# Optimization experiments

Measured on AMD Instinct MI355X. Metric: run time of the kernel, lower is better.

Reference implementation:

```python
import jax, jax.numpy as jnp
import numpy as np
import math

N_NODES = 20000
N_EDGES = 320000
NODE_IN = 128
HIDDEN = 64
HEADS = 4
TIME_DIM = 64
SCALE = 60.0 / 1.0  # sensitivity / epsilon


def _linear_params(key, din, dout):
    k1, k2 = jax.random.split(key)
    bound = 1.0 / math.sqrt(din)
    w = jax.random.uniform(k1, (din, dout), minval=-bound, maxval=bound, dtype=jnp.float32)
    b = jax.random.uniform(k2, (dout,), minval=-bound, maxval=bound, dtype=jnp.float32)
    return w, b


def setup_inputs() -> dict:
    key = jax.random.key(0)
    ks = jax.random.split(key, 16)
    edge_index = jax.random.randint(ks[0], (2, N_EDGES), 0, N_NODES, dtype=jnp.int64)
    raw_time = jax.random.uniform(ks[1], (N_EDGES, 1), dtype=jnp.float32) * 86400.0
    noise = jax.random.laplace(ks[2], (N_EDGES, 1), dtype=jnp.float32) * SCALE
    node_emb = jax.random.normal(ks[3], (N_NODES, NODE_IN), dtype=jnp.float32)
    HC = HEADS * HIDDEN
    wq1, bq1 = _linear_params(ks[4], NODE_IN, HC)
    wk1, bk1 = _linear_params(ks[5], NODE_IN, HC)
    wv1, bv1 = _linear_params(ks[6], NODE_IN, HC)
    wt1, bt1 = _linear_params(ks[7], TIME_DIM, HC)
    wq2, bq2 = _linear_params(ks[8], HC, HC)
    wk2, bk2 = _linear_params(ks[9], HC, HC)
    wv2, bv2 = _linear_params(ks[10], HC, HC)
    wt2, bt2 = _linear_params(ks[11], TIME_DIM, HC)
    wc, bc = _linear_params(ks[12], HC, 1)
    return dict(edge_index=edge_index, raw_time=raw_time, noise=noise, node_emb=node_emb,
                wq1=wq1, bq1=bq1, wk1=wk1, bk1=bk1, wv1=wv1, bv1=bv1, wt1=wt1, bt1=bt1,
                wq2=wq2, bq2=bq2, wk2=wk2, bk2=bk2, wv2=wv2, bv2=bv2, wt2=wt2, bt2=bt2,
                wc=wc, bc=bc)


def time_encode(t):
    # t: [E, 1] -> [E, TIME_DIM]; interleaved sin/cos as in TimeEncoder
    half = jnp.arange(0, TIME_DIM, 2, dtype=jnp.float32)
    div_term = jnp.exp(half * (-math.log(10000.0) / TIME_DIM))  # [TIME_DIM/2]
    arg = t * div_term  # [E, TIME_DIM/2]
    te = jnp.stack([jnp.sin(arg), jnp.cos(arg)], axis=-1)  # [E, T/2, 2]
    return te.reshape(t.shape[0], TIME_DIM)


def temporal_conv(x, src, dst, time_enc, wq, bq, wk, bk, wv, bv, wt, bt):
    # gather-QKV, edge softmax over dst segments, scatter-add aggregation
    N = x.shape[0]
    q = (x @ wq + bq).reshape(N, HEADS, HIDDEN)
    k = (x @ wk + bk).reshape(N, HEADS, HIDDEN)
    v = (x @ wv + bv).reshape(N, HEADS, HIDDEN)
    t_enc = (time_enc @ wt + bt).reshape(-1, HEADS, HIDDEN)  # [E,H,C]
    q_i = q[dst]                      # [E,H,C]
    k_j = k[src] + t_enc              # [E,H,C]
    alpha = (q_i * k_j).sum(-1) / math.sqrt(HIDDEN)  # [E,H]
    # segment softmax over index = dst (PyG softmax semantics)
    amax = jax.ops.segment_max(alpha, dst, num_segments=N)  # [N,H]
    ea = jnp.exp(alpha - amax[dst])
    denom = jax.ops.segment_sum(ea, dst, num_segments=N)
    alpha = ea / (denom[dst] + 1e-16)
    msg = v[src] * alpha[..., None]   # [E,H,C]
    out = jax.ops.segment_sum(msg, dst, num_segments=N)  # [N,H,C]
    return out.reshape(N, HEADS * HIDDEN)


def reference(edge_index, raw_time, noise, node_emb,
              wq1, bq1, wk1, bk1, wv1, bv1, wt1, bt1,
              wq2, bq2, wk2, bk2, wv2, bv2, wt2, bt2,
              wc, bc):
    src, dst = edge_index[0], edge_index[1]
    noisy_time = raw_time + noise                 # Laplace mechanism
    time_encoded = time_encode(noisy_time)        # [E, TIME_DIM]
    x = jax.nn.relu(temporal_conv(node_emb, src, dst, time_encoded,
                                  wq1, bq1, wk1, bk1, wv1, bv1, wt1, bt1))
    x = jax.nn.relu(temporal_conv(x, src, dst, time_encoded,
                                  wq2, bq2, wk2, bk2, wv2, bv2, wt2, bt2))
    edge_emb = x[src] + x[dst]                    # [E, H*C]
    out = edge_emb @ wc + bc                      # [E, 1]
    return out.squeeze(-1)
```

## Files before the change

kernel.cpp:

```cpp
#include <hip/hip_runtime.h>
#include <hip/hip_fp16.h>
#include <math.h>

#define NN   20000
#define NE   320000
#define NIN  128
#define HC   256
#define NB   1024

#define AGG_BLOCKS 2500
#define AGG_STRIDE 10000
#define LOG2E_8    0.18033688f

#define GEMM_BLOCKS 1280
#define GEMM_RT     157

typedef unsigned short u16;
typedef __attribute__((ext_vector_type(8))) short bf16x8;
typedef __attribute__((ext_vector_type(4))) float f32x4;

__device__ __forceinline__ float bf2f(u16 u) {
  union { unsigned int i; float f; } x;
  x.i = ((unsigned int)u) << 16;
  return x.f;
}
__device__ __forceinline__ u16 f2bf(float f) {
  union { float f; unsigned int i; } x;
  x.f = f;
  unsigned int r = x.i + 0x7fffu + ((x.i >> 16) & 1u);
  return (u16)(r >> 16);
}
__device__ __forceinline__ float bflo(int v) {
  union { int i; float f; } x; x.i = v << 16; return x.f;
}
__device__ __forceinline__ float bfhi(int v) {
  union { int i; float f; } x; x.i = v & 0xffff0000; return x.f;
}

__device__ __forceinline__ float ldf(const void* p, int i, bool fbf) {
  return fbf ? bf2f(((const u16*)p)[i]) : ((const float*)p)[i];
}
__device__ __forceinline__ int ldsrc(const void* p, int e, bool is64) {
  const int* p32 = (const int*)p;
  return is64 ? p32[2 * e] : p32[e];
}
__device__ __forceinline__ int lddst(const void* p, int e, bool is64) {
  const int* p32 = (const int*)p;
  return is64 ? p32[2 * (NE + e)] : p32[NE + e];
}
__device__ __forceinline__ void stout(void* p, int i, float v, bool fbf) {
  if (fbf) ((u16*)p)[i] = f2bf(v);
  else ((float*)p)[i] = v;
}

__device__ __forceinline__ void gload_lds16(const u16* g, u16* l) {
  __builtin_amdgcn_global_load_lds(
      (const __attribute__((address_space(1))) void*)g,
      (__attribute__((address_space(3))) void*)l, 16, 0, 0);
}

__device__ __forceinline__ float dpp_row_allsum(float s) {
  union fi { float f; int i; };
  fi a, b;
  a.f = s;
  b.i = __builtin_amdgcn_update_dpp(0, a.i, 0x121, 0xf, 0xf, true); a.f += b.f;
  b.i = __builtin_amdgcn_update_dpp(0, a.i, 0x122, 0xf, 0xf, true); a.f += b.f;
  b.i = __builtin_amdgcn_update_dpp(0, a.i, 0x124, 0xf, 0xf, true); a.f += b.f;
  b.i = __builtin_amdgcn_update_dpp(0, a.i, 0x128, 0xf, 0xf, true); a.f += b.f;
  return a.f;
}

__device__ __forceinline__ float fexp2(float x) {
#if __has_builtin(__builtin_amdgcn_exp2f)
  return __builtin_amdgcn_exp2f(x);
#else
  return exp2f(x);
#endif
}

#if __has_builtin(__builtin_amdgcn_fdot2_f32_bf16)
#define HAS_BF16_DOT2 1
typedef __attribute__((ext_vector_type(2))) __bf16 bfv2_t;
__device__ __forceinline__ float qkdot2(int a, int b, float c) {
  return __builtin_amdgcn_fdot2_f32_bf16(__builtin_bit_cast(bfv2_t, a),
                                         __builtin_bit_cast(bfv2_t, b), c, false);
}
#else
#define HAS_BF16_DOT2 0
#endif

__device__ __forceinline__ void edge_do(int2 kk, int2 vv, float tt, int2 q2,
    float dc0, float dc1,
    float qsx, float qsy, float qsz, float qsw,
    float px, float py, float pz, float pw, float qb,
    float& denom, float& a0, float& a1, float& a2, float& a3) {
  const float CH = 0.15915494f;
  const float CL = (float)(0.15915494309189535 - (double)0.15915494f);
  float x0 = tt * dc0, x1 = tt * dc1;
  float p0 = x0 * CH, p1 = x1 * CH;
  float e0 = fmaf(x0, CH, -p0), e1 = fmaf(x1, CH, -p1);
  e0 = fmaf(x0, CL, e0);  e1 = fmaf(x1, CL, e1);
  float fr0 = (p0 - rintf(p0)) + e0;
  float fr1 = (p1 - rintf(p1)) + e1;
  float sv0 = __builtin_amdgcn_sinf(fr0), cv0 = __builtin_amdgcn_cosf(fr0);
  float sv1 = __builtin_amdgcn_sinf(fr1), cv1 = __builtin_amdgcn_cosf(fr1);
  float stp = sv0 * px + cv0 * py + sv1 * pz + cv1 * pw;
#if HAS_BF16_DOT2
  float sqk = qkdot2(kk.y, q2.y, qkdot2(kk.x, q2.x, 0.f));
  float partial = sqk * LOG2E_8 + stp;
#else
  float partial = stp + qsx * bflo(kk.x) + qsy * bfhi(kk.x) +
                  qsz * bflo(kk.y) + qsw * bfhi(kk.y);
#endif
  float a = dpp_row_allsum(partial) + qb;
  float ea = fexp2(a);
  denom += ea;
  a0 = fmaf(ea, bflo(vv.x), a0);
  a1 = fmaf(ea, bfhi(vv.x), a1);
  a2 = fmaf(ea, bflo(vv.y), a2);
  a3 = fmaf(ea, bfhi(vv.y), a3);
}

__global__ void devinit_kernel(const void* __restrict__ eidx,
                               const void* __restrict__ nemb,
                               int* __restrict__ flags, float* __restrict__ divt) {
  int lane = threadIdx.x;
  if (lane < 32) {
    const float c32 = (float)(-0.14391156831212787);
    float prod = (float)(2 * lane) * c32;
    divt[lane] = (float)exp((double)prod);
  }
  if (lane == 0) {
    const int* p32 = (const int*)eidx;
    int is64 = 1;
    for (int i = 1; i < 128; i += 2)
      if (p32[i] != 0) { is64 = 0; break; }
    const u16* q16 = (const u16*)nemb;
    int fbf = 1;
    for (int i = 0; i < 128; i += 2) {
      unsigned e = (q16[i] >> 7) & 0xFF;
      if (e < 90 || e > 140) { fbf = 0; break; }
    }
    flags[0] = is64;
    flags[1] = fbf;
  }
}

__global__ void sentinel_kernel(const int* __restrict__ flags, void* __restrict__ out) {
  int i = blockIdx.x * 256 + threadIdx.x;
  if (i < NE) stout(out, i, 3000.0f, flags[1] != 0);
}
__global__ void raw_sentinel_kernel(u16* __restrict__ out) {
  int i = blockIdx.x * 256 + threadIdx.x;
  if (i < NE) out[i] = f2bf(3000.0f);
}

__global__ void zero_kernel(int* __restrict__ p, int n) {
  int i = blockIdx.x * 256 + threadIdx.x;
  if (i < n) p[i] = 0;
}

__global__ void hist_kernel(const int* __restrict__ flags, const void* __restrict__ eidx,
                            int* __restrict__ cnt) {
  bool is64 = flags[0] != 0;
  int e = blockIdx.x * 256 + threadIdx.x;
  if (e < NE) {
    int d = lddst(eidx, e, is64);
    if ((unsigned)d < NN) atomicAdd(&cnt[d], 1);
  }
}

__global__ void scan1_kernel(const int* __restrict__ cnt, int* __restrict__ offs,
                             int* __restrict__ bsum, int n) {
  __shared__ int s[256];
  int b = blockIdx.x, t = threadIdx.x, i = b * 256 + t;
  int x = (i < n) ? cnt[i] : 0;
  s[t] = x;
  __syncthreads();
  for (int off = 1; off < 256; off <<= 1) {
    int y = (t >= off) ? s[t - off] : 0;
    __syncthreads();
    s[t] += y;
    __syncthreads();
  }
  if (i < n) offs[i] = s[t] - x;
  if (t == 255) bsum[b] = s[t];
}

__global__ void scan2_kernel(int* __restrict__ bsum, int* __restrict__ offs,
                             int nb, int n) {
  __shared__ int s[256];
  int t = threadIdx.x;
  int x = (t < nb) ? bsum[t] : 0;
  s[t] = x;
  __syncthreads();
  for (int off = 1; off < 256; off <<= 1) {
    int y = (t >= off) ? s[t - off] : 0;
    __syncthreads();
    s[t] += y;
    __syncthreads();
  }
  if (t < nb) bsum[t] = s[t] - x;
  if (t == 255) offs[n] = s[t];
}

__global__ void scan3_kernel(int* __restrict__ offs, const int* __restrict__ bsum,
                             int* __restrict__ cursor, int n) {
  int i = blockIdx.x * 256 + threadIdx.x;
  if (i < n) {
    int v = offs[i] + bsum[blockIdx.x];
    offs[i] = v;
    cursor[i] = v;
  }
}

__global__ void fill_kernel(const int* __restrict__ flags, const void* __restrict__ eidx,
                            const void* __restrict__ rawt, const void* __restrict__ noise,
                            int* __restrict__ cursor, int* __restrict__ ssrc,
                            float* __restrict__ stt) {
  bool is64 = flags[0] != 0, fbf = flags[1] != 0;
  int e = blockIdx.x * 256 + threadIdx.x;
  if (e < NE) {
    int d = lddst(eidx, e, is64);
    if ((unsigned)d < NN) {
      int pos = atomicAdd(&cursor[d], 1);
      if ((unsigned)pos < NE) {
        int src = ldsrc(eidx, e, is64);
        if ((unsigned)src >= NN) src = 0;
        ssrc[pos] = src;
        stt[pos] = ldf(rawt, e, fbf) + ldf(noise, e, fbf);
      }
    }
  }
}

__global__ __launch_bounds__(256) void cast_kernel(const int* __restrict__ flags,
                                                   const void* __restrict__ in,
                                                   u16* __restrict__ out) {
  if (flags[1]) return;
  int i = blockIdx.x * 256 + threadIdx.x;
  if (i < NN * NIN / 4) {
    float4 v = ((const float4*)in)[i];
    ushort4 o;
    o.x = f2bf(v.x); o.y = f2bf(v.y); o.z = f2bf(v.z); o.w = f2bf(v.w);
    ((ushort4*)out)[i] = o;
  }
}

__global__ void transw3_kernel(const int* __restrict__ flags, const void* __restrict__ W0,
                               const void* __restrict__ W1, const void* __restrict__ W2,
                               u16* __restrict__ WtBig, int K) {
  bool fbf = flags[1] != 0;
  __shared__ u16 tile[64][65];
  int z = blockIdx.z;
  const void* W = (z == 0) ? W0 : (z == 1) ? W1 : W2;
  u16* dst = WtBig + (size_t)z * 256 * K;
  int kb = blockIdx.x * 64, cb = blockIdx.y * 64;
  int tx = threadIdx.x & 63, ty = threadIdx.x >> 6;
  for (int i = ty; i < 64; i += 4)
    tile[tx][i] = f2bf(ldf(W, (kb + i) * HC + cb + tx, fbf));
  __syncthreads();
  for (int i = ty; i < 64; i += 4)
    dst[(size_t)(cb + i) * K + kb + tx] = tile[i][tx];
}

__global__ void wcombbias_kernel(const int* __restrict__ flags, const void* __restrict__ wt,
                                 const u16* __restrict__ Wqt, u16* __restrict__ Wout,
                                 const void* __restrict__ bq, const void* __restrict__ bk,
                                 const void* __restrict__ bv, float* __restrict__ biasBig,
                                 int K) {
  bool fbf = flags[1] != 0;
  int b = blockIdx.x, t = threadIdx.x;
  if (b < 256) {
    __shared__ float wrow[64];
    int j = b, h = j >> 6;
    if (t < 64) wrow[t] = ldf(wt, (j & 63) * HC + h * 64 + t, fbf);
    __syncthreads();
    if (t < K) {
      float s = 0.f;
#pragma unroll 8
      for (int mm = 0; mm < 64; ++mm)
        s += wrow[mm] * bf2f(Wqt[(size_t)(h * 64 + mm) * K + t]);
      Wout[(size_t)j * K + t] = f2bf(s);
    }
  } else if (b < 259) {
    int bb = b - 256;
    const void* p = (bb == 0) ? bq : (bb == 1) ? bk : bv;
    biasBig[bb * 256 + t] = ldf(p, t, fbf);
  } else {
    int j = t, h = j >> 6;
    float s = 0.f;
    for (int mm = 0; mm < 64; ++mm)
      s += ldf(bq, h * 64 + mm, fbf) * ldf(wt, (j & 63) * HC + h * 64 + mm, fbf);
    biasBig[768 + j] = s;
  }
}

template <bool AWS>
__global__ __launch_bounds__(256) void gemm_mfma(
    const int* __restrict__ flags, const void* __restrict__ Ap,
    const u16* __restrict__ Acast, const u16* __restrict__ Wt,
    const float* __restrict__ bias, u16* __restrict__ C, int M, int K) {
  bool fbf = flags[1] != 0;
  const u16* A = AWS ? (const u16*)Ap : (fbf ? (const u16*)Ap : Acast);

  int lid = blockIdx.x;
  int xcd = lid & 7;
  int j = lid >> 3;
  int rl = j >> 3, col = j & 7;
  const int qr = GEMM_RT >> 3, rem = GEMM_RT & 7;
  int nrows = qr + (xcd < rem ? 1 : 0);
  if (rl >= nrows) return;
  int row = xcd * qr + (xcd < rem ? xcd : rem) + rl;
  int rb = row * 128, cb = col * 128;

  __shared__ u16 As[2][128 * 32];
  __shared__ u16 Bs[2][128 * 32];
  int tid = threadIdx.x;
  int wave = tid >> 6, lane = tid & 63;
  int l15 = lane & 15, quad = lane >> 4;
  int mbase = (wave >> 1) * 64, nbase = (wave & 1) * 64;

  f32x4 acc[4][4];
#pragma unroll
  for (int mt = 0; mt < 4; ++mt)
#pragma unroll
    for (int nt = 0; nt < 4; ++nt)
#pragma unroll
      for (int r = 0; r < 4; ++r) acc[mt][nt][r] = 0.f;

  int srow0 = tid >> 2, schunk0 = tid & 3;
  int srow1 = (tid + 256) >> 2, schunk1 = (tid + 256) & 3;
  int gchunk0 = schunk0 ^ (srow0 & 3);
  int gchunk1 = schunk1 ^ (srow1 & 3);
  int arow0 = rb + srow0; if (arow0 >= M) arow0 = M - 1;
  int arow1 = rb + srow1; if (arow1 >= M) arow1 = M - 1;
  int slo0 = srow0 * 32 + schunk0 * 8;
  int slo1 = srow1 * 32 + schunk1 * 8;
  const u16* bsrc0 = Wt + (size_t)(cb + srow0) * K + gchunk0 * 8;
  const u16* bsrc1 = Wt + (size_t)(cb + srow1) * K + gchunk1 * 8;
  const u16* asrc0 = A + (size_t)arow0 * K + gchunk0 * 8;
  const u16* asrc1 = A + (size_t)arow1 * K + gchunk1 * 8;

  auto STAGE = [&](int b, int kk) {
    gload_lds16(asrc0 + kk, &As[b][slo0]);
    gload_lds16(asrc1 + kk, &As[b][slo1]);
    gload_lds16(bsrc0 + kk, &Bs[b][slo0]);
    gload_lds16(bsrc1 + kk, &Bs[b][slo1]);
  };

  auto COMPUTE = [&](int b) {
    bf16x8 bfrag[4];
#pragma unroll
    for (int nt = 0; nt < 4; ++nt) {
      int col2 = nbase + nt * 16 + l15;
      bfrag[nt] = *(const bf16x8*)&Bs[b][col2 * 32 + ((quad ^ (col2 & 3)) * 8)];
    }
#pragma unroll
    for (int mt = 0; mt < 4; ++mt) {
      int row2 = mbase + mt * 16 + l15;
      bf16x8 afrag = *(const bf16x8*)&As[b][row2 * 32 + ((quad ^ (row2 & 3)) * 8)];
#pragma unroll
      for (int nt = 0; nt < 4; ++nt)
        acc[mt][nt] = __builtin_amdgcn_mfma_f32_16x16x32_bf16(afrag, bfrag[nt], acc[mt][nt], 0, 0, 0);
    }
  };

  STAGE(0, 0);
  __syncthreads();
  int cur = 0;
  for (int kk = 32; kk < K; kk += 32) {
    STAGE(cur ^ 1, kk);
    COMPUTE(cur);
    __syncthreads();
    cur ^= 1;
  }
  COMPUTE(cur);

  float bvv[4];
#pragma unroll
  for (int nt = 0; nt < 4; ++nt) bvv[nt] = bias[cb + nbase + nt * 16 + l15];
#pragma unroll
  for (int mt = 0; mt < 4; ++mt) {
#pragma unroll
    for (int r = 0; r < 4; ++r) {
      int grow = rb + mbase + mt * 16 + quad * 4 + r;
      if (grow < M) {
        size_t rowo = (size_t)grow * NB + cb + nbase + l15;
#pragma unroll
        for (int nt = 0; nt < 4; ++nt)
          C[rowo + nt * 16] = f2bf(acc[mt][nt][r] + bvv[nt]);
      }
    }
  }
}

template <int DOY>
__global__ __launch_bounds__(256) void aggfused_kernel(
    const int* __restrict__ flags, const int* __restrict__ ssrc,
    const int* __restrict__ offsets, const float* __restrict__ stt,
    const float* __restrict__ divt,
    const u16* __restrict__ qkvp, const void* __restrict__ bt,
    u16* __restrict__ xout, const void* __restrict__ wc,
    float* __restrict__ ynode) {
  bool fbf = flags[1] != 0;
  int lane = threadIdx.x & 63;
  int c = lane * 4;

  int i0 = (2 * lane) & 31;
  float dc0 = divt[i0], dc1 = divt[i0 + 1];
  float btv0 = ldf(bt, c + 0, fbf), btv1 = ldf(bt, c + 1, fbf);
  float btv2 = ldf(bt, c + 2, fbf), btv3 = ldf(bt, c + 3, fbf);
  float wcv0 = 0.f, wcv1 = 0.f, wcv2 = 0.f, wcv3 = 0.f;
  if (DOY) {
    wcv0 = ldf(wc, c + 0, fbf); wcv1 = ldf(wc, c + 1, fbf);
    wcv2 = ldf(wc, c + 2, fbf); wcv3 = ldf(wc, c + 3, fbf);
  }

  int n = blockIdx.x * 4 + (threadIdx.x >> 6);
  int s0 = offsets[n], s1 = offsets[n + 1];
  int2 q2 = *(const int2*)(qkvp + (size_t)n * NB + c);
  int2 p2 = *(const int2*)(qkvp + (size_t)n * NB + 768 + c);

  while (n < NN) {
    int n1 = n + AGG_STRIDE;
    int n1c = (n1 < NN) ? n1 : 0;
    int s0n = offsets[n1c], s1n = offsets[n1c + 1];
    int2 q2n = *(const int2*)(qkvp + (size_t)n1c * NB + c);
    int2 p2n = *(const int2*)(qkvp + (size_t)n1c * NB + 768 + c);

    float qx = bflo(q2.x), qy = bfhi(q2.x), qz = bflo(q2.y), qw = bfhi(q2.y);
    float px = bflo(p2.x) * LOG2E_8, py = bfhi(p2.x) * LOG2E_8;
    float pz = bflo(p2.y) * LOG2E_8, pw = bfhi(p2.y) * LOG2E_8;
    float pb = qx * btv0 + qy * btv1 + qz * btv2 + qw * btv3;
    float qb = dpp_row_allsum(pb) * LOG2E_8;
    float qsx = qx * LOG2E_8, qsy = qy * LOG2E_8;
    float qsz = qz * LOG2E_8, qsw = qw * LOG2E_8;

    float denom = 0.f, acc0 = 0.f, acc1 = 0.f, acc2 = 0.f, acc3 = 0.f;
    const int* sp = ssrc + s0;
    const float* tp = stt + s0;
    int ecnt = s1 - s0;
    int e = 0;
    if (ecnt >= 4) {
      int sA = sp[0], sB = sp[1], sC = sp[2], sD = sp[3];
      while (e + 4 <= ecnt) {
        const u16* bA = qkvp + ((unsigned)sA << 10) + c;
        const u16* bB = qkvp + ((unsigned)sB << 10) + c;
        const u16* bC = qkvp + ((unsigned)sC << 10) + c;
        const u16* bD = qkvp + ((unsigned)sD << 10) + c;
        int2 kA = *(const int2*)(bA + 256), vA = *(const int2*)(bA + 512);
        int2 kB = *(const int2*)(bB + 256), vB = *(const int2*)(bB + 512);
        int2 kC = *(const int2*)(bC + 256), vC = *(const int2*)(bC + 512);
        int2 kD = *(const int2*)(bD + 256), vD = *(const int2*)(bD + 512);
        float ttA = tp[e], ttB = tp[e + 1], ttC = tp[e + 2], ttD = tp[e + 3];
        int en = e + 4;
        if (en + 4 <= ecnt) {
          sA = sp[en]; sB = sp[en + 1]; sC = sp[en + 2]; sD = sp[en + 3];
        }
        edge_do(kA, vA, ttA, q2, dc0, dc1, qsx, qsy, qsz, qsw, px, py, pz, pw, qb,
                denom, acc0, acc1, acc2, acc3);
        edge_do(kB, vB, ttB, q2, dc0, dc1, qsx, qsy, qsz, qsw, px, py, pz, pw, qb,
                denom, acc0, acc1, acc2, acc3);
        edge_do(kC, vC, ttC, q2, dc0, dc1, qsx, qsy, qsz, qsw, px, py, pz, pw, qb,
                denom, acc0, acc1, acc2, acc3);
        edge_do(kD, vD, ttD, q2, dc0, dc1, qsx, qsy, qsz, qsw, px, py, pz, pw, qb,
                denom, acc0, acc1, acc2, acc3);
        e = en;
      }
    }
    for (; e < ecnt; ++e) {
      int s = sp[e];
      const u16* bS = qkvp + ((unsigned)s << 10) + c;
      int2 kS = *(const int2*)(bS + 256), vS = *(const int2*)(bS + 512);
      float tt = tp[e];
      edge_do(kS, vS, tt, q2, dc0, dc1, qsx, qsy, qsz, qsw, px, py, pz, pw, qb,
              denom, acc0, acc1, acc2, acc3);
    }

    float inv = 1.f / (denom + 1e-16f);
    ushort4 r;
    r.x = f2bf(fmaxf(acc0 * inv, 0.f));
    r.y = f2bf(fmaxf(acc1 * inv, 0.f));
    r.z = f2bf(fmaxf(acc2 * inv, 0.f));
    r.w = f2bf(fmaxf(acc3 * inv, 0.f));
    *(ushort4*)(xout + (size_t)n * HC + c) = r;
    if (DOY) {
      float yv = bf2f(r.x) * wcv0 + bf2f(r.y) * wcv1 +
                 bf2f(r.z) * wcv2 + bf2f(r.w) * wcv3;
      yv = dpp_row_allsum(yv);
      yv += __shfl_xor(yv, 16);
      yv += __shfl_xor(yv, 32);
      if (lane == 0) ynode[n] = yv;
    }

    n = n1;
    s0 = s0n; s1 = s1n; q2 = q2n; p2 = p2n;
  }
}

__global__ __launch_bounds__(256) void final2_kernel(
    const int* __restrict__ flags, const void* __restrict__ eidx,
    const float* __restrict__ y, const void* __restrict__ bc,
    void* __restrict__ out) {
  bool is64 = flags[0] != 0, fbf = flags[1] != 0;
  int e = blockIdx.x * 256 + threadIdx.x;
  if (e >= NE) return;
  int src = ldsrc(eidx, e, is64);
  int dst = lddst(eidx, e, is64);
  if ((unsigned)src >= NN) src = 0;
  if ((unsigned)dst >= NN) dst = 0;
  stout(out, e, y[src] + y[dst] + ldf(bc, 0, fbf), fbf);
}

extern "C" void kernel_launch(void* const* d_in, const int* in_sizes, int n_in,
                              void* d_out, int out_size, void* d_ws, size_t ws_size,
                              hipStream_t stream) {
  const void* eidx  = d_in[0];
  const void* rawt  = d_in[1];
  const void* noise = d_in[2];
  const void* nemb  = d_in[3];
  const void *wq1 = d_in[4],  *bq1 = d_in[5];
  const void *wk1 = d_in[6],  *bk1 = d_in[7];
  const void *wv1 = d_in[8],  *bv1 = d_in[9];
  const void *wt1 = d_in[10], *bt1 = d_in[11];
  const void *wq2 = d_in[12], *bq2 = d_in[13];
  const void *wk2 = d_in[14], *bk2 = d_in[15];
  const void *wv2 = d_in[16], *bv2 = d_in[17];
  const void *wt2 = d_in[18], *bt2 = d_in[19];
  const void *wcp = d_in[20], *bcp = d_in[21];

  char* ws = (char*)d_ws;
  size_t off = 0;
  auto alloc = [&](size_t bytes) -> void* {
    void* p = ws + off;
    off += (bytes + 255) & ~(size_t)255;
    return p;
  };
  int*   flags  = (int*)alloc(256);
  float* divt   = (float*)alloc(256);
  u16*   WtBig  = (u16*)alloc((size_t)NB * HC * 2);
  float* biasBig= (float*)alloc((size_t)NB * 4);
  u16*   qkvp   = (u16*)alloc((size_t)NN * NB * 2);
  u16*   x1     = (u16*)alloc((size_t)NN * HC * 2);
  u16*   x2     = (u16*)alloc((size_t)NN * HC * 2);
  u16*   acast  = (u16*)alloc((size_t)NN * NIN * 2);
  float* ynode  = (float*)alloc((size_t)NN * 4);
  int* offsets  = (int*)alloc((size_t)(NN + 1) * 4);
  int* cursor   = (int*)alloc((size_t)NN * 4);
  int* bsum     = (int*)alloc(256 * 4);
  int* ssrc     = (int*)alloc((size_t)NE * 4);
  float* stt    = (float*)alloc((size_t)NE * 4);
  size_t need = off;

  int gN = (NN + 255) / 256, gE = (NE + 255) / 256;
  int nb = (NN + 255) / 256;

  if (ws_size < 1024) {
    raw_sentinel_kernel<<<gE, 256, 0, stream>>>((u16*)d_out);
    return;
  }
  devinit_kernel<<<1, 64, 0, stream>>>(eidx, nemb, flags, divt);
  if (need > ws_size) {
    sentinel_kernel<<<gE, 256, 0, stream>>>(flags, d_out);
    return;
  }

  zero_kernel<<<gN, 256, 0, stream>>>(cursor, NN);
  hist_kernel<<<gE, 256, 0, stream>>>(flags, eidx, cursor);
  scan1_kernel<<<nb, 256, 0, stream>>>(cursor, offsets, bsum, NN);
  scan2_kernel<<<1, 256, 0, stream>>>(bsum, offsets, nb, NN);
  scan3_kernel<<<nb, 256, 0, stream>>>(offsets, bsum, cursor, NN);
  fill_kernel<<<gE, 256, 0, stream>>>(flags, eidx, rawt, noise, cursor, ssrc, stt);

  cast_kernel<<<(NN * NIN / 4 + 255) / 256, 256, 0, stream>>>(flags, nemb, acast);

  dim3 gt1(NIN / 64, 4, 3), gt2(HC / 64, 4, 3);

  transw3_kernel<<<gt1, 256, 0, stream>>>(flags, wq1, wk1, wv1, WtBig, NIN);
  wcombbias_kernel<<<260, 256, 0, stream>>>(flags, wt1, WtBig, WtBig + (size_t)768 * NIN,
                                            bq1, bk1, bv1, biasBig, NIN);
  gemm_mfma<false><<<GEMM_BLOCKS, 256, 0, stream>>>(flags, nemb, acast, WtBig, biasBig,
                                                    qkvp, NN, NIN);
  aggfused_kernel<0><<<AGG_BLOCKS, 256, 0, stream>>>(flags, ssrc, offsets, stt, divt,
                                                     qkvp, bt1, x1, wcp, ynode);

  transw3_kernel<<<gt2, 256, 0, stream>>>(flags, wq2, wk2, wv2, WtBig, HC);
  wcombbias_kernel<<<260, 256, 0, stream>>>(flags, wt2, WtBig, WtBig + (size_t)768 * HC,
                                            bq2, bk2, bv2, biasBig, HC);
  gemm_mfma<true><<<GEMM_BLOCKS, 256, 0, stream>>>(flags, x1, (const u16*)0, WtBig, biasBig,
                                                   qkvp, NN, HC);
  aggfused_kernel<1><<<AGG_BLOCKS, 256, 0, stream>>>(flags, ssrc, offsets, stt, divt,
                                                     qkvp, bt2, x2, wcp, ynode);

  final2_kernel<<<gE, 256, 0, stream>>>(flags, eidx, ynode, bcp, d_out);
}
```

Baseline: 326.5 us.

## Fuse preprocessing kernels, single-block scan, and full-K LDS staging in GEMM

Merges zeroing into the init kernel, fuses the destination histogram with the fp32-to-bf16 cast, and replaces the three-kernel prefix scan with one 1024-thread block scan. This removes several small kernel launches and their dependencies. The GEMM now takes K as a template parameter and stages 128-wide K slices into larger LDS buffers, loading all of them before computing, instead of using a 32-wide double buffer. That cuts barriers but loses load/compute overlap and raises LDS use to 64KB per block, which may lower occupancy.

```diff
diff --git a/kernel.cpp b/kernel.cpp
--- a/kernel.cpp
+++ b/kernel.cpp
@@ -121,28 +121,33 @@
   a3 = fmaf(ea, bfhi(vv.y), a3);
 }
 
-__global__ void devinit_kernel(const void* __restrict__ eidx,
-                               const void* __restrict__ nemb,
-                               int* __restrict__ flags, float* __restrict__ divt) {
-  int lane = threadIdx.x;
-  if (lane < 32) {
-    const float c32 = (float)(-0.14391156831212787);
-    float prod = (float)(2 * lane) * c32;
-    divt[lane] = (float)exp((double)prod);
-  }
-  if (lane == 0) {
-    const int* p32 = (const int*)eidx;
-    int is64 = 1;
-    for (int i = 1; i < 128; i += 2)
-      if (p32[i] != 0) { is64 = 0; break; }
-    const u16* q16 = (const u16*)nemb;
-    int fbf = 1;
-    for (int i = 0; i < 128; i += 2) {
-      unsigned e = (q16[i] >> 7) & 0xFF;
-      if (e < 90 || e > 140) { fbf = 0; break; }
-    }
-    flags[0] = is64;
-    flags[1] = fbf;
+__global__ void devinit_zero_kernel(const void* __restrict__ eidx,
+                                    const void* __restrict__ nemb,
+                                    int* __restrict__ flags, float* __restrict__ divt,
+                                    int* __restrict__ cursor) {
+  int i = blockIdx.x * 256 + threadIdx.x;
+  if (i < NN) cursor[i] = 0;
+  if (blockIdx.x == 0) {
+    int lane = threadIdx.x;
+    if (lane < 32) {
+      const float c32 = (float)(-0.14391156831212787);
+      float prod = (float)(2 * lane) * c32;
+      divt[lane] = (float)exp((double)prod);
+    }
+    if (lane == 0) {
+      const int* p32 = (const int*)eidx;
+      int is64 = 1;
+      for (int k = 1; k < 128; k += 2)
+        if (p32[k] != 0) { is64 = 0; break; }
+      const u16* q16 = (const u16*)nemb;
+      int fbf = 1;
+      for (int k = 0; k < 128; k += 2) {
+        unsigned e = (q16[k] >> 7) & 0xFF;
+        if (e < 90 || e > 140) { fbf = 0; break; }
+      }
+      flags[0] = is64;
+      flags[1] = fbf;
+    }
   }
 }
 
@@ -155,63 +160,61 @@
   if (i < NE) out[i] = f2bf(3000.0f);
 }
 
-__global__ void zero_kernel(int* __restrict__ p, int n) {
-  int i = blockIdx.x * 256 + threadIdx.x;
-  if (i < n) p[i] = 0;
-}
-
-__global__ void hist_kernel(const int* __restrict__ flags, const void* __restrict__ eidx,
-                            int* __restrict__ cnt) {
+__global__ void hist_cast_kernel(const int* __restrict__ flags, const void* __restrict__ eidx,
+                                 int* __restrict__ cnt, const void* __restrict__ nemb,
+                                 u16* __restrict__ acast) {
   bool is64 = flags[0] != 0;
-  int e = blockIdx.x * 256 + threadIdx.x;
-  if (e < NE) {
+  int b = blockIdx.x, t = threadIdx.x;
+  if (b < (NE / 256)) {
+    int e = b * 256 + t;
     int d = lddst(eidx, e, is64);
     if ((unsigned)d < NN) atomicAdd(&cnt[d], 1);
   }
-}
-
-__global__ void scan1_kernel(const int* __restrict__ cnt, int* __restrict__ offs,
-                             int* __restrict__ bsum, int n) {
-  __shared__ int s[256];
-  int b = blockIdx.x, t = threadIdx.x, i = b * 256 + t;
-  int x = (i < n) ? cnt[i] : 0;
-  s[t] = x;
+  if (!flags[1]) {
+    int i = b * 256 + t;
+    if (i < NN * NIN / 4) {
+      float4 v = ((const float4*)nemb)[i];
+      ushort4 o;
+      o.x = f2bf(v.x); o.y = f2bf(v.y); o.z = f2bf(v.z); o.w = f2bf(v.w);
+      ((ushort4*)acast)[i] = o;
+    }
+  }
+}
+
+__global__ __launch_bounds__(1024) void scanall_kernel(int* __restrict__ cnt_cursor,
+                                                       int* __restrict__ offs) {
+  __shared__ int s[1024];
+  int t = threadIdx.x;
+  const int PER = (NN + 1023) / 1024;
+  int base = t * PER;
+  int loc[PER];
+  int sum = 0;
+#pragma unroll
+  for (int i = 0; i < PER; ++i) {
+    int idx = base + i;
+    int v = (idx < NN) ? cnt_cursor[idx] : 0;
+    loc[i] = sum;
+    sum += v;
+  }
+  s[t] = sum;
   __syncthreads();
-  for (int off = 1; off < 256; off <<= 1) {
+  for (int off = 1; off < 1024; off <<= 1) {
     int y = (t >= off) ? s[t - off] : 0;
     __syncthreads();
     s[t] += y;
     __syncthreads();
   }
-  if (i < n) offs[i] = s[t] - x;
-  if (t == 255) bsum[b] = s[t];
-}
-
-__global__ void scan2_kernel(int* __restrict__ bsum, int* __restrict__ offs,
-                             int nb, int n) {
-  __shared__ int s[256];
-  int t = threadIdx.x;
-  int x = (t < nb) ? bsum[t] : 0;
-  s[t] = x;
-  __syncthreads();
-  for (int off = 1; off < 256; off <<= 1) {
-    int y = (t >= off) ? s[t - off] : 0;
-    __syncthreads();
-    s[t] += y;
-    __syncthreads();
-  }
-  if (t < nb) bsum[t] = s[t] - x;
-  if (t == 255) offs[n] = s[t];
-}
-
-__global__ void scan3_kernel(int* __restrict__ offs, const int* __restrict__ bsum,
-                             int* __restrict__ cursor, int n) {
-  int i = blockIdx.x * 256 + threadIdx.x;
-  if (i < n) {
-    int v = offs[i] + bsum[blockIdx.x];
-    offs[i] = v;
-    cursor[i] = v;
-  }
+  int tbase = s[t] - sum;
+#pragma unroll
+  for (int i = 0; i < PER; ++i) {
+    int idx = base + i;
+    if (idx < NN) {
+      int v = tbase + loc[i];
+      offs[idx] = v;
+      cnt_cursor[idx] = v;
+    }
+  }
+  if (t == 1023) offs[NN] = s[t];
 }
 
 __global__ void fill_kernel(const int* __restrict__ flags, const void* __restrict__ eidx,
@@ -231,19 +234,6 @@
         stt[pos] = ldf(rawt, e, fbf) + ldf(noise, e, fbf);
       }
     }
-  }
-}
-
-__global__ __launch_bounds__(256) void cast_kernel(const int* __restrict__ flags,
-                                                   const void* __restrict__ in,
-                                                   u16* __restrict__ out) {
-  if (flags[1]) return;
-  int i = blockIdx.x * 256 + threadIdx.x;
-  if (i < NN * NIN / 4) {
-    float4 v = ((const float4*)in)[i];
-    ushort4 o;
-    o.x = f2bf(v.x); o.y = f2bf(v.y); o.z = f2bf(v.z); o.w = f2bf(v.w);
-    ((ushort4*)out)[i] = o;
   }
 }
 
@@ -296,11 +286,11 @@
   }
 }
 
-template <bool AWS>
+template <int KT, bool AWS>
 __global__ __launch_bounds__(256) void gemm_mfma(
     const int* __restrict__ flags, const void* __restrict__ Ap,
     const u16* __restrict__ Acast, const u16* __restrict__ Wt,
-    const float* __restrict__ bias, u16* __restrict__ C, int M, int K) {
+    const float* __restrict__ bias, u16* __restrict__ C, int M) {
   bool fbf = flags[1] != 0;
   const u16* A = AWS ? (const u16*)Ap : (fbf ? (const u16*)Ap : Acast);
 
@@ -314,8 +304,8 @@
   int row = xcd * qr + (xcd < rem ? xcd : rem) + rl;
   int rb = row * 128, cb = col * 128;
 
-  __shared__ u16 As[2][128 * 32];
-  __shared__ u16 Bs[2][128 * 32];
+  __shared__ u16 As[128 * 128];
+  __shared__ u16 Bs[128 * 128];
   int tid = threadIdx.x;
   int wave = tid >> 6, lane = tid & 63;
   int l15 = lane & 15, quad = lane >> 4;
@@ -337,45 +327,43 @@
   int arow1 = rb + srow1; if (arow1 >= M) arow1 = M - 1;
   int slo0 = srow0 * 32 + schunk0 * 8;
   int slo1 = srow1 * 32 + schunk1 * 8;
-  const u16* bsrc0 = Wt + (size_t)(cb + srow0) * K + gchunk0 * 8;
-  const u16* bsrc1 = Wt + (size_t)(cb + srow1) * K + gchunk1 * 8;
-  const u16* asrc0 = A + (size_t)arow0 * K + gchunk0 * 8;
-  const u16* asrc1 = A + (size_t)arow1 * K + gchunk1 * 8;
-
-  auto STAGE = [&](int b, int kk) {
-    gload_lds16(asrc0 + kk, &As[b][slo0]);
-    gload_lds16(asrc1 + kk, &As[b][slo1]);
-    gload_lds16(bsrc0 + kk, &Bs[b][slo0]);
-    gload_lds16(bsrc1 + kk, &Bs[b][slo1]);
-  };
-
-  auto COMPUTE = [&](int b) {
-    bf16x8 bfrag[4];
-#pragma unroll
-    for (int nt = 0; nt < 4; ++nt) {
-      int col2 = nbase + nt * 16 + l15;
-      bfrag[nt] = *(const bf16x8*)&Bs[b][col2 * 32 + ((quad ^ (col2 & 3)) * 8)];
-    }
-#pragma unroll
-    for (int mt = 0; mt < 4; ++mt) {
-      int row2 = mbase + mt * 16 + l15;
-      bf16x8 afrag = *(const bf16x8*)&As[b][row2 * 32 + ((quad ^ (row2 & 3)) * 8)];
-#pragma unroll
-      for (int nt = 0; nt < 4; ++nt)
-        acc[mt][nt] = __builtin_amdgcn_mfma_f32_16x16x32_bf16(afrag, bfrag[nt], acc[mt][nt], 0, 0, 0);
-    }
-  };
-
-  STAGE(0, 0);
-  __syncthreads();
-  int cur = 0;
-  for (int kk = 32; kk < K; kk += 32) {
-    STAGE(cur ^ 1, kk);
-    COMPUTE(cur);
+  const u16* bsrc0 = Wt + (size_t)(cb + srow0) * KT + gchunk0 * 8;
+  const u16* bsrc1 = Wt + (size_t)(cb + srow1) * KT + gchunk1 * 8;
+  const u16* asrc0 = A + (size_t)arow0 * KT + gchunk0 * 8;
+  const u16* asrc1 = A + (size_t)arow1 * KT + gchunk1 * 8;
+
+#pragma unroll
+  for (int sl = 0; sl < KT / 128; ++sl) {
+    if (sl) __syncthreads();
+#pragma unroll
+    for (int s = 0; s < 4; ++s) {
+      int kk = sl * 128 + s * 32;
+      int sb = s * 4096;
+      gload_lds16(asrc0 + kk, &As[sb + slo0]);
+      gload_lds16(asrc1 + kk, &As[sb + slo1]);
+      gload_lds16(bsrc0 + kk, &Bs[sb + slo0]);
+      gload_lds16(bsrc1 + kk, &Bs[sb + slo1]);
+    }
     __syncthreads();
-    cur ^= 1;
-  }
-  COMPUTE(cur);
+#pragma unroll
+    for (int s = 0; s < 4; ++s) {
+      int sb = s * 4096;
+      bf16x8 bfrag[4];
+#pragma unroll
+      for (int nt = 0; nt < 4; ++nt) {
+        int col2 = nbase + nt * 16 + l15;
+        bfrag[nt] = *(const bf16x8*)&Bs[sb + col2 * 32 + ((quad ^ (col2 & 3)) * 8)];
+      }
+#pragma unroll
+      for (int mt = 0; mt < 4; ++mt) {
+        int row2 = mbase + mt * 16 + l15;
+        bf16x8 afrag = *(const bf16x8*)&As[sb + row2 * 32 + ((quad ^ (row2 & 3)) * 8)];
+#pragma unroll
+        for (int nt = 0; nt < 4; ++nt)
+          acc[mt][nt] = __builtin_amdgcn_mfma_f32_16x16x32_bf16(afrag, bfrag[nt], acc[mt][nt], 0, 0, 0);
+      }
+    }
+  }
 
   float bvv[4];
 #pragma unroll
@@ -548,48 +536,42 @@
   float* ynode  = (float*)alloc((size_t)NN * 4);
   int* offsets  = (int*)alloc((size_t)(NN + 1) * 4);
   int* cursor   = (int*)alloc((size_t)NN * 4);
-  int* bsum     = (int*)alloc(256 * 4);
   int* ssrc     = (int*)alloc((size_t)NE * 4);
   float* stt    = (float*)alloc((size_t)NE * 4);
   size_t need = off;
 
   int gN = (NN + 255) / 256, gE = (NE + 255) / 256;
-  int nb = (NN + 255) / 256;
 
   if (ws_size < 1024) {
     raw_sentinel_kernel<<<gE, 256, 0, stream>>>((u16*)d_out);
     return;
   }
-  devinit_kernel<<<1, 64, 0, stream>>>(eidx, nemb, flags, divt);
+  devinit_zero_kernel<<<gN, 256, 0, stream>>>(eidx, nemb, flags, divt, cursor);
   if (need > ws_size) {
     sentinel_kernel<<<gE, 256, 0, stream>>>(flags, d_out);
     return;
   }
 
-  zero_kernel<<<gN, 256, 0, stream>>>(cursor, NN);
-  hist_kernel<<<gE, 256, 0, stream>>>(flags, eidx, cursor);
-  scan1_kernel<<<nb, 256, 0, stream>>>(cursor, offsets, bsum, NN);
-  scan2_kernel<<<1, 256, 0, stream>>>(bsum, offsets, nb, NN);
-  scan3_kernel<<<nb, 256, 0, stream>>>(offsets, bsum, cursor, NN);
+  hist_cast_kernel<<<(NN * NIN / 4 + 255) / 256, 256, 0, stream>>>(flags, eidx, cursor,
+                                                                   nemb, acast);
+  scanall_kernel<<<1, 1024, 0, stream>>>(cursor, offsets);
   fill_kernel<<<gE, 256, 0, stream>>>(flags, eidx, rawt, noise, cursor, ssrc, stt);
-
-  cast_kernel<<<(NN * NIN / 4 + 255) / 256, 256, 0, stream>>>(flags, nemb, acast);
 
   dim3 gt1(NIN / 64, 4, 3), gt2(HC / 64, 4, 3);
 
   transw3_kernel<<<gt1, 256, 0, stream>>>(flags, wq1, wk1, wv1, WtBig, NIN);
   wcombbias_kernel<<<260, 256, 0, stream>>>(flags, wt1, WtBig, WtBig + (size_t)768 * NIN,
                                             bq1, bk1, bv1, biasBig, NIN);
-  gemm_mfma<false><<<GEMM_BLOCKS, 256, 0, stream>>>(flags, nemb, acast, WtBig, biasBig,
-                                                    qkvp, NN, NIN);
+  gemm_mfma<NIN, false><<<GEMM_BLOCKS, 256, 0, stream>>>(flags, nemb, acast, WtBig,
+                                                         biasBig, qkvp, NN);
   aggfused_kernel<0><<<AGG_BLOCKS, 256, 0, stream>>>(flags, ssrc, offsets, stt, divt,
                                                      qkvp, bt1, x1, wcp, ynode);
 
   transw3_kernel<<<gt2, 256, 0, stream>>>(flags, wq2, wk2, wv2, WtBig, HC);
   wcombbias_kernel<<<260, 256, 0, stream>>>(flags, wt2, WtBig, WtBig + (size_t)768 * HC,
                                             bq2, bk2, bv2, biasBig, HC);
-  gemm_mfma<true><<<GEMM_BLOCKS, 256, 0, stream>>>(flags, x1, (const u16*)0, WtBig, biasBig,
-                                                   qkvp, NN, HC);
+  gemm_mfma<HC, true><<<GEMM_BLOCKS, 256, 0, stream>>>(flags, x1, (const u16*)0, WtBig,
+                                                       biasBig, qkvp, NN);
   aggfused_kernel<1><<<AGG_BLOCKS, 256, 0, stream>>>(flags, ssrc, offsets, stt, divt,
                                                      qkvp, bt2, x2, wcp, ynode);
 
```

Measured after the change: 338.7 us. +3.7%, slower.
